# Performance work log

Hardware: AMD Instinct MI355X
Metric: run time of the kernel (lower is better)

Reference implementation:

```python
import jax, jax.numpy as jnp
import numpy as np

B, S, H, DH, D, FD, FU = 4, 256, 12, 64, 768, 2048, 2048


def setup_inputs() -> dict:
    key = jax.random.key(0)
    ks = jax.random.split(key, 12)
    s = 0.02  # typical init scale for weights
    return {
        "resid_pre": jax.random.normal(ks[0], (B, S, D), jnp.float32),
        "ln_scale": jax.random.uniform(ks[1], (B, S, 1), jnp.float32, 0.5, 2.0),
        "probs": jax.nn.softmax(jax.random.normal(ks[2], (B, H, S, S), jnp.float32), axis=-1),
        "W_O": jax.random.normal(ks[3], (H, DH, D), jnp.float32) * s,
        "W_V": jax.random.normal(ks[4], (H, D, DH), jnp.float32) * s,
        "enc_W": jax.random.normal(ks[5], (FD, D), jnp.float32) * s,
        "enc_b": jax.random.normal(ks[6], (FD,), jnp.float32) * s,
        "b_dec": jax.random.normal(ks[7], (D,), jnp.float32) * s,
        "up_dec_W": jax.random.normal(ks[8], (D, FU), jnp.float32) * s,
        "up_b_dec": jax.random.normal(ks[9], (D,), jnp.float32) * s,
        "pruned_features": jax.random.normal(ks[10], (B, S, FU), jnp.float32),
        "connection_mask": jax.random.randint(ks[11], (FD, FU), 0, 2, jnp.int32),
    }


def reference(resid_pre, ln_scale, probs, W_O, W_V, enc_W, enc_b, b_dec,
              up_dec_W, up_b_dec, pruned_features, connection_mask):
    # W_OV: [h, d_model(in), d_model(out)]
    W_OV = jnp.einsum('hko,hmk->hmo', W_O, W_V)
    mask = connection_mask.astype(resid_pre.dtype)

    # --- initial contributions ---
    act_ln = resid_pre / ln_scale                                  # [b,s,d]
    pre_moving = jnp.einsum('bsi,hio,fo->bshf', act_ln, W_OV, enc_W)  # [b,s,h,f_down]
    approx = jnp.einsum('bhqk,bkhf->bqf', probs, pre_moving)       # [b,q,f_down]

    # --- pruned contributions (one upstream AE) ---
    virtual = jnp.einsum('fo,hio,iu->hfu', enc_W, W_OV, up_dec_W) * mask[None]
    up_ln = pruned_features / ln_scale                             # [b,k,f_up]
    post_ov = jnp.einsum('bku,hfu->bhkf', up_ln, virtual)          # [b,h,k,f_down]
    approx = approx + jnp.einsum('bhqk,bhkf->bqf', probs, post_ov)

    # --- bias terms ---
    approx = approx + enc_b[None, None] - (enc_W @ b_dec)[None, None]
    ub_ln = up_b_dec[None, None] / ln_scale                        # [b,s,d]
    ub_post = jnp.einsum('hmd,bsm->bsd', W_OV, ub_ln)              # attn path through OV
    approx = approx + jnp.einsum('fd,bsd->bsf', enc_W, ub_post)
    return approx
```

## Files before the change

kernel.cpp:

```cpp
#include <hip/hip_runtime.h>
#include <hip/hip_bf16.h>
#include <stdint.h>

typedef __bf16 bf16;
typedef __bf16 bf16x8 __attribute__((ext_vector_type(8)));
typedef __bf16 bf16x4 __attribute__((ext_vector_type(4)));
typedef float f32x4 __attribute__((ext_vector_type(4)));

#define AS1 __attribute__((address_space(1)))
#define AS3 __attribute__((address_space(3)))


__device__ __forceinline__ void gld16(const bf16* g, bf16* l) {
  __builtin_amdgcn_global_load_lds((AS1 void*)g, (AS3 void*)l, 16, 0, 0);
}

__global__ void k_sentinel(float* __restrict__ out) {
  int i = blockIdx.x * 256 + threadIdx.x;
  if (i < 2097152) out[i] = 1048576.0f;
}

__global__ void k_prep(const float* __restrict__ lns, float* __restrict__ invln,
                       const float* __restrict__ enc_W, bf16* __restrict__ encWb,
                       const float* __restrict__ probs, bf16* __restrict__ probsT,
                       const int* __restrict__ cmask, bf16* __restrict__ maskb,
                       const float* __restrict__ W_O, bf16* __restrict__ WOb,
                       const float* __restrict__ resid, bf16* __restrict__ Xb,
                       bf16* __restrict__ BgTail, long ldTail) {
  const int bid = blockIdx.x, t = threadIdx.x;
  if (bid < 1) {
    for (int k = 0; k < 4; k++) { int j = t + k * 256; invln[j] = 1.0f / lns[j]; }
  } else if (bid < 1537) {
    long idx = ((long)(bid - 1) * 256 + t) * 4;
    float4 v = *(const float4*)(enc_W + idx);
    bf16x4 o; o[0]=(bf16)v.x; o[1]=(bf16)v.y; o[2]=(bf16)v.z; o[3]=(bf16)v.w;
    *(bf16x4*)(encWb + idx) = o;
  } else if (bid < 4609) {
    long idx = ((long)(bid - 1537) * 256 + t) * 4;
    int s = (int)(idx & 255), q = (int)((idx >> 8) & 255);
    int hb = (int)(idx >> 16), h = hb % 12, b = hb / 12;
    float4 v = *(const float4*)(probs + idx);
    bf16x4 o; o[0]=(bf16)v.x; o[1]=(bf16)v.y; o[2]=(bf16)v.z; o[3]=(bf16)v.w;
    *(bf16x4*)(probsT + (long)b * 786432 + (long)q * 3072 + h * 256 + s) = o;
  } else if (bid < 8705) {
    long idx = ((long)(bid - 4609) * 256 + t) * 4;
    int4 v = *(const int4*)(cmask + idx);
    bf16x4 o; o[0]=(bf16)(float)v.x; o[1]=(bf16)(float)v.y;
    o[2]=(bf16)(float)v.z; o[3]=(bf16)(float)v.w;
    *(bf16x4*)(maskb + idx) = o;
  } else if (bid < 9857) {
    long idx = ((long)(bid - 8705) * 256 + t) * 4;
    int o = (int)(idx % 768), r = (int)((idx / 768) & 127), h = (int)(idx / (768 * 128));
    bf16x4 ov;
    if (r < 64) {
      float4 v = *(const float4*)(W_O + (long)(h * 64 + r) * 768 + o);
      ov[0]=(bf16)v.x; ov[1]=(bf16)v.y; ov[2]=(bf16)v.z; ov[3]=(bf16)v.w;
    } else { ov[0]=ov[1]=ov[2]=ov[3]=(bf16)0.0f; }
    *(bf16x4*)(WOb + idx) = ov;
  } else if (bid < 10625) {
    long idx = ((long)(bid - 9857) * 256 + t) * 4;
    float il = 1.0f / lns[idx / 768];
    float4 v = *(const float4*)(resid + idx);
    bf16x4 o; o[0]=(bf16)(v.x*il); o[1]=(bf16)(v.y*il);
    o[2]=(bf16)(v.z*il); o[3]=(bf16)(v.w*il);
    *(bf16x4*)(Xb + idx) = o;
  } else {
    long idx = ((long)(bid - 10625) * 256 + t) * 4;
    int f = (int)(idx / 768), d = (int)(idx % 768);
    float4 v = *(const float4*)(enc_W + idx);
    bf16x4 o; o[0]=(bf16)v.x; o[1]=(bf16)v.y; o[2]=(bf16)v.z; o[3]=(bf16)v.w;
    *(bf16x4*)(BgTail + (long)f * ldTail + d) = o;
  }
}

__global__ void k_prepT(const float* __restrict__ wv, bf16* __restrict__ WVt,
                        const float* __restrict__ wo, bf16* __restrict__ W_Ot,
                        const float* __restrict__ updW, bf16* __restrict__ updWt,
                        const float* __restrict__ pr, const float* __restrict__ lns,
                        bf16* __restrict__ Ut) {
  __shared__ float tile[32][33];
  const int bid = blockIdx.x;
  int lane = threadIdx.x & 31, rg = threadIdx.x >> 5;
  if (bid < 1152) {
    int r0 = bid;
    int x = r0 % 4, y = (r0 / 4) % 24, h = r0 / 96;
    int k0 = x * 32, i0 = y * 32;
    if (k0 < 64) {
      for (int r = rg; r < 32; r += 8)
        tile[r][lane] = wv[((long)(h * 768 + i0 + r)) * 64 + k0 + lane];
      __syncthreads();
      for (int r = rg; r < 32; r += 8)
        WVt[((long)h * 128 + k0 + r) * 768 + i0 + lane] = (bf16)tile[lane][r];
    } else {
      for (int r = rg; r < 32; r += 8)
        WVt[((long)h * 128 + k0 + r) * 768 + i0 + lane] = (bf16)0.0f;
    }
  } else if (bid < 1728) {
    int r0 = bid - 1152;
    int x = r0 % 2, y = (r0 / 2) % 24, h = r0 / 48;
    int k0 = x * 32, o0 = y * 32;
    for (int r = rg; r < 32; r += 8)
      tile[r][lane] = wo[((long)(h * 64 + k0 + r)) * 768 + o0 + lane];
    __syncthreads();
    for (int r = rg; r < 32; r += 8)
      W_Ot[((long)(h * 768 + o0 + r)) * 64 + k0 + lane] = (bf16)tile[lane][r];
  } else if (bid < 3264) {
    int r0 = bid - 1728;
    int u0 = (r0 % 64) * 32, i0 = (r0 / 64) * 32;
    for (int r = rg; r < 32; r += 8)
      tile[r][lane] = updW[((long)(i0 + r)) * 2048 + u0 + lane];
    __syncthreads();
    for (int r = rg; r < 32; r += 8)
      updWt[((long)(u0 + r)) * 768 + i0 + lane] = (bf16)tile[lane][r];
  } else {
    int r0 = bid - 3264;
    int u0 = (r0 % 64) * 32, s0 = ((r0 / 64) % 8) * 32, b = r0 / 512;
    for (int r = rg; r < 32; r += 8) {
      int s = s0 + r;
      tile[r][lane] = pr[((long)(b * 256 + s)) * 2048 + u0 + lane] *
                      (1.0f / lns[b * 256 + s]);
    }
    __syncthreads();
    for (int r = rg; r < 32; r += 8)
      Ut[((long)b * 2048 + u0 + r) * 256 + s0 + lane] = (bf16)tile[lane][r];
  }
}

__global__ void k_sred(const float* __restrict__ Sp, bf16* __restrict__ dst, long ldd) {
  int i = blockIdx.x * 256 + threadIdx.x;
  if (i < 196608) {
    long idx = (long)i * 4;
    int m = (int)(idx / 768), o = (int)(idx % 768);
    float4 v = *(const float4*)(Sp + idx);
    float4 a = *(const float4*)(Sp + 786432 + idx);
    float4 b = *(const float4*)(Sp + 2 * 786432 + idx);
    float4 c = *(const float4*)(Sp + 3 * 786432 + idx);
    v.x += a.x + b.x + c.x; v.y += a.y + b.y + c.y;
    v.z += a.z + b.z + c.z; v.w += a.w + b.w + c.w;
    bf16x4 ov;
    ov[0] = (bf16)v.x; ov[1] = (bf16)v.y; ov[2] = (bf16)v.z; ov[3] = (bf16)v.w;
    *(bf16x4*)(dst + (long)m * ldd + o) = ov;
  }
}


__device__ __forceinline__ float blk_reduce(float s) {
  __shared__ float red[256];
  red[threadIdx.x] = s; __syncthreads();
  for (int o = 128; o > 0; o >>= 1) {
    if ((int)threadIdx.x < o) red[threadIdx.x] += red[threadIdx.x + o];
    __syncthreads();
  }
  float r = red[0]; __syncthreads();
  return r;
}

__global__ void k_bias_t(const float* __restrict__ W_V, const float* __restrict__ up_b,
                         float* __restrict__ t_hk) {
  int j = blockIdx.x, h = j >> 6, k = j & 63;
  float s = 0.f;
  for (int m = threadIdx.x; m < 768; m += 256)
    s += W_V[((long)(h * 768 + m)) * 64 + k] * up_b[m];
  float r = blk_reduce(s);
  if (threadIdx.x == 0) t_hk[j] = r;
}

__global__ void k_bias_w(const float* __restrict__ W_O, const float* __restrict__ t_hk,
                         float* __restrict__ w) {
  int d = blockIdx.x;
  float s = 0.f;
  for (int j = threadIdx.x; j < 768; j += 256)
    s += W_O[(long)j * 768 + d] * t_hk[j];
  float r = blk_reduce(s);
  if (threadIdx.x == 0) w[d] = r;
}

__global__ void k_bias_c(const float* __restrict__ enc_W, const float* __restrict__ enc_b,
                         const float* __restrict__ b_dec, const float* __restrict__ w,
                         float* __restrict__ c0, float* __restrict__ c1) {
  int f = blockIdx.x;
  float s0 = 0.f, s1 = 0.f;
  for (int d = threadIdx.x; d < 768; d += 256) {
    float e = enc_W[(long)f * 768 + d];
    s0 += e * b_dec[d];
    s1 += e * w[d];
  }
  float r0 = blk_reduce(s0);
  float r1 = blk_reduce(s1);
  if (threadIdx.x == 0) { c0[f] = enc_b[f] - r0; c1[f] = r1; }
}

__global__ __launch_bounds__(256)
void gemm_bt(const bf16* __restrict__ A, const bf16* __restrict__ B, void* __restrict__ Cv,
             int M, int N, int K,
             long lda, long ldb, long ldc,
             int batchH,
             long sa_b, long sa_h, long sb_b, long sb_h, long sc_b, long sc_h,
             int mode, int kChunk,
             const bf16* __restrict__ mask, long mask_ld)
{
  __shared__ __align__(16) bf16 Asm[128 * 64];
  __shared__ __align__(16) bf16 Bsm[128 * 64];

  const int t = threadIdx.x;

  const int nbx = gridDim.x, nby = gridDim.y;
  const int nxy = nbx * nby;
  int orig = blockIdx.x + nbx * blockIdx.y;
  int qq = nxy >> 3, rr = nxy & 7;
  int xcd = orig & 7, lid = orig >> 3;
  int swz = (xcd < rr) ? (xcd * (qq + 1) + lid)
                       : (rr * (qq + 1) + (xcd - rr) * qq + lid);
  const int m0 = (swz % nby) * 128;
  const int n0 = (swz / nby) * 128;

  long aoff, boff, coff;
  int k0, k1;
  if (mode == 4) {
    int z = blockIdx.z;
    int bb = z / batchH, kc = z - bb * batchH;
    aoff = (long)bb * sa_b;
    boff = (long)bb * sb_b;
    coff = (long)bb * sc_b + (long)kc * sc_h;
    k0 = kc * kChunk; k1 = k0 + kChunk; if (k1 > K) k1 = K;
  } else if (mode >= 2) {
    int z = blockIdx.z;
    aoff = 0; boff = 0;
    coff = (long)z * (long)M * ldc;
    k0 = z * kChunk; k1 = k0 + kChunk; if (k1 > K) k1 = K;
  } else {
    int z = blockIdx.z;
    int bb = z / batchH, hh = z - bb * batchH;
    aoff = (long)bb * sa_b + (long)hh * sa_h;
    boff = (long)bb * sb_b + (long)hh * sb_h;
    coff = (long)bb * sc_b + (long)hh * sc_h;
    k0 = 0; k1 = K;
  }

  const bf16* Ab = A + aoff + (long)m0 * lda;
  const bf16* Bb = B + boff + (long)n0 * ldb;

  const int r0 = t >> 3;
  const int g8 = t & 7;

  const int L = t & 63, w = t >> 6;
  const int wm = (w & 1) * 64, wn = (w >> 1) * 64;
  const int r16 = L & 15, q = L >> 4;

  f32x4 acc[4][4];
#pragma unroll
  for (int i = 0; i < 4; i++)
#pragma unroll
    for (int j = 0; j < 4; j++) acc[i][j] = (f32x4){0.f, 0.f, 0.f, 0.f};

  for (int kt = k0; kt < k1; kt += 64) {
#pragma unroll
    for (int j = 0; j < 4; j++) {
      int row = j * 32 + r0;
      int sc = ((g8 ^ (row & 7)) << 3);
      gld16(Ab + (long)row * lda + (kt + sc), &Asm[j * 2048 + t * 8]);
      gld16(Bb + (long)row * ldb + (kt + sc), &Bsm[j * 2048 + t * 8]);
    }
    __syncthreads();

#pragma unroll
    for (int h2 = 0; h2 < 2; h2++) {
      bf16x8 af[4], bfr[4];
#pragma unroll
      for (int i = 0; i < 4; i++) {
        int ra = wm + i * 16 + r16;
        af[i]  = *(const bf16x8*)&Asm[ra * 64 + ((((h2 << 2) + q) ^ (ra & 7)) << 3)];
        int rb = wn + i * 16 + r16;
        bfr[i] = *(const bf16x8*)&Bsm[rb * 64 + ((((h2 << 2) + q) ^ (rb & 7)) << 3)];
      }
#pragma unroll
      for (int mi = 0; mi < 4; mi++)
#pragma unroll
        for (int ni = 0; ni < 4; ni++)
          acc[mi][ni] = __builtin_amdgcn_mfma_f32_16x16x32_bf16(af[mi], bfr[ni], acc[mi][ni], 0, 0, 0);
    }
    __syncthreads();
  }

  if (mode >= 2) {
    float* C = (float*)Cv;
#pragma unroll
    for (int mi = 0; mi < 4; mi++)
#pragma unroll
      for (int ni = 0; ni < 4; ni++)
#pragma unroll
        for (int r = 0; r < 4; r++) {
          int gm = m0 + wm + mi * 16 + q * 4 + r;
          int gn = n0 + wn + ni * 16 + r16;
          long idx = coff + (long)gm * ldc + gn;
          float v = acc[mi][ni][r];
          if (mode == 3) v += C[idx];
          C[idx] = v;
        }
  } else {
    bf16* C = (bf16*)Cv;
#pragma unroll
    for (int mi = 0; mi < 4; mi++)
#pragma unroll
      for (int ni = 0; ni < 4; ni++)
#pragma unroll
        for (int r = 0; r < 4; r++) {
          int gm = m0 + wm + mi * 16 + q * 4 + r;
          int gn = n0 + wn + ni * 16 + r16;
          float v = acc[mi][ni][r];
          if (mode == 1) v *= (float)mask[(long)gm * mask_ld + gn];
          C[coff + (long)gm * ldc + gn] = (bf16)v;
        }
  }
}

__global__ __launch_bounds__(512, 2)
void gemm_fp2(const bf16* __restrict__ A, const bf16* __restrict__ B,
              float* __restrict__ C,
              int M, int N, int K, long lda, long ldb, long ldc,
              int mode, int kChunk)
{
  __shared__ __align__(16) bf16 SM[2][2][16384];

  const int t = threadIdx.x;

  const int nz = gridDim.z;
  int fid = blockIdx.x + gridDim.x * (blockIdx.y + gridDim.y * blockIdx.z);
  const int z  = fid % nz;
  const int t2 = fid / nz;
  const int m0 = (t2 >> 3) * 256;
  const int n0 = (t2 & 7) * 256;

  const long coff = (long)z * (long)M * ldc;
  int k0 = z * kChunk, k1 = k0 + kChunk; if (k1 > K) k1 = K;
  const int NT = (k1 > k0) ? (k1 - k0) >> 6 : 0;

  const bf16* Ab = A + (long)m0 * lda + k0;
  const bf16* Bb = B + (long)n0 * ldb + k0;

  const int sr = t >> 3;
  const int g8 = t & 7;

  const int L = t & 63, w = t >> 6;
  const int wm = (w & 1) * 128;
  const int wn = (w >> 1) * 64;
  const int r16 = L & 15, q = L >> 4;

  f32x4 acc[8][4];
#pragma unroll
  for (int i = 0; i < 8; i++)
#pragma unroll
    for (int j = 0; j < 4; j++) acc[i][j] = (f32x4){0.f, 0.f, 0.f, 0.f};

  auto stage = [&](int tt, int buf) {
    const bf16* Ap = Ab + (long)tt * 64;
    const bf16* Bp = Bb + (long)tt * 64;
#pragma unroll
    for (int j = 0; j < 4; j++) {
      int row = j * 64 + sr;
      int sc = ((g8 ^ (row & 7)) << 3);
      gld16(Ap + (long)row * lda + sc, &SM[buf][0][j * 4096 + t * 8]);
    }
#pragma unroll
    for (int j = 0; j < 4; j++) {
      int row = j * 64 + sr;
      int sc = ((g8 ^ (row & 7)) << 3);
      gld16(Bp + (long)row * ldb + sc, &SM[buf][1][j * 4096 + t * 8]);
    }
  };

  if (NT >= 1) stage(0, 0);

  for (int tt = 0; tt < NT; tt++) {
    if (tt + 1 < NT) {
      stage(tt + 1, (tt + 1) & 1);
      asm volatile("s_waitcnt vmcnt(8)" ::: "memory");
    } else {
      asm volatile("s_waitcnt vmcnt(0)" ::: "memory");
    }
    __builtin_amdgcn_s_barrier();

    const bf16* As = &SM[tt & 1][0][0];
    const bf16* Bs = &SM[tt & 1][1][0];

    bf16x8 a0[4], a1[4], bq0[4], bq1[4];
#pragma unroll
    for (int i = 0; i < 4; i++) {
      int ra = wm + i * 16 + r16;
      a0[i] = *(const bf16x8*)&As[ra * 64 + ((q ^ (ra & 7)) << 3)];
    }
#pragma unroll
    for (int i = 0; i < 4; i++) {
      int rb = wn + i * 16 + r16;
      bq0[i] = *(const bf16x8*)&Bs[rb * 64 + ((q ^ (rb & 7)) << 3)];
    }
#pragma unroll
    for (int i = 0; i < 4; i++) {
      int ra = wm + (4 + i) * 16 + r16;
      a1[i] = *(const bf16x8*)&As[ra * 64 + ((q ^ (ra & 7)) << 3)];
    }
    __builtin_amdgcn_sched_barrier(0);
    __builtin_amdgcn_s_setprio(1);
#pragma unroll
    for (int mi = 0; mi < 4; mi++)
#pragma unroll
      for (int ni = 0; ni < 4; ni++)
        acc[mi][ni] = __builtin_amdgcn_mfma_f32_16x16x32_bf16(a0[mi], bq0[ni], acc[mi][ni], 0, 0, 0);
    __builtin_amdgcn_s_setprio(0);
#pragma unroll
    for (int i = 0; i < 4; i++) {
      int ra = wm + i * 16 + r16;
      a0[i] = *(const bf16x8*)&As[ra * 64 + (((4 + q) ^ (ra & 7)) << 3)];
    }
#pragma unroll
    for (int i = 0; i < 4; i++) {
      int rb = wn + i * 16 + r16;
      bq1[i] = *(const bf16x8*)&Bs[rb * 64 + (((4 + q) ^ (rb & 7)) << 3)];
    }
    __builtin_amdgcn_sched_barrier(0);
    __builtin_amdgcn_s_setprio(1);
#pragma unroll
    for (int mi = 0; mi < 4; mi++)
#pragma unroll
      for (int ni = 0; ni < 4; ni++)
        acc[4 + mi][ni] = __builtin_amdgcn_mfma_f32_16x16x32_bf16(a1[mi], bq0[ni], acc[4 + mi][ni], 0, 0, 0);
    __builtin_amdgcn_s_setprio(0);
#pragma unroll
    for (int i = 0; i < 4; i++) {
      int ra = wm + (4 + i) * 16 + r16;
      a1[i] = *(const bf16x8*)&As[ra * 64 + (((4 + q) ^ (ra & 7)) << 3)];
    }
    __builtin_amdgcn_sched_barrier(0);
    __builtin_amdgcn_s_setprio(1);
#pragma unroll
    for (int mi = 0; mi < 4; mi++)
#pragma unroll
      for (int ni = 0; ni < 4; ni++)
        acc[mi][ni] = __builtin_amdgcn_mfma_f32_16x16x32_bf16(a0[mi], bq1[ni], acc[mi][ni], 0, 0, 0);
    __builtin_amdgcn_s_setprio(0);
    __builtin_amdgcn_sched_barrier(0);
    __builtin_amdgcn_s_setprio(1);
#pragma unroll
    for (int mi = 0; mi < 4; mi++)
#pragma unroll
      for (int ni = 0; ni < 4; ni++)
        acc[4 + mi][ni] = __builtin_amdgcn_mfma_f32_16x16x32_bf16(a1[mi], bq1[ni], acc[4 + mi][ni], 0, 0, 0);
    __builtin_amdgcn_s_setprio(0);

    __builtin_amdgcn_s_barrier();
  }

#pragma unroll
  for (int mi = 0; mi < 8; mi++)
#pragma unroll
    for (int ni = 0; ni < 4; ni++)
#pragma unroll
      for (int r = 0; r < 4; r++) {
        int gm = m0 + wm + mi * 16 + q * 4 + r;
        int gn = n0 + wn + ni * 16 + r16;
        long idx = coff + (long)gm * ldc + gn;
        float v = acc[mi][ni][r];
        if (mode == 3) v += C[idx];
        C[idx] = v;
      }
}

__global__ void k_out(const float* __restrict__ Cp, const float* __restrict__ c0,
                      const float* __restrict__ c1, const float* __restrict__ invln,
                      float* __restrict__ out, int nsplit) {
  int i4 = blockIdx.x * 256 + threadIdx.x;
  long i = (long)i4 * 4;
  int n = (int)(i & 2047), m = (int)(i >> 11);
  float4 v = *(const float4*)(Cp + i);
  for (int z = 1; z < nsplit; z++) {
    float4 u = *(const float4*)(Cp + i + (long)z * 2097152);
    v.x += u.x; v.y += u.y; v.z += u.z; v.w += u.w;
  }
  float il = invln[m];
  float4 a = *(const float4*)(c0 + n);
  float4 b = *(const float4*)(c1 + n);
  v.x += a.x + b.x * il;
  v.y += a.y + b.y * il;
  v.z += a.z + b.z * il;
  v.w += a.w + b.w * il;
  *(float4*)(out + i) = v;
}


extern "C" void kernel_launch(void* const* d_in, const int* in_sizes, int n_in,
                              void* d_out, int out_size, void* d_ws, size_t ws_size,
                              hipStream_t stream) {
  (void)out_size;
  float* out = (float*)d_out;

  int iresid = -1, iln = -1, iprobs = -1, iencb = -1, ipruned = -1, imask = -1;
  int iwo = -1, iwv = -1, iencw = -1, iupdw = -1, ibdec = -1, iupb = -1;
  for (int i = 0; i < n_in; i++) {
    switch (in_sizes[i]) {
      case 786432:  iresid  = i; break;
      case 1024:    iln     = i; break;
      case 3145728: iprobs  = i; break;
      case 2048:    iencb   = i; break;
      case 2097152: ipruned = i; break;
      case 4194304: imask   = i; break;
      case 589824:  if (iwo   < 0) iwo   = i; else iwv   = i; break;
      case 1572864: if (iencw < 0) iencw = i; else iupdw = i; break;
      case 768:     if (ibdec < 0) ibdec = i; else iupb  = i; break;
      default: break;
    }
  }
  bool ok = n_in == 12 && iresid >= 0 && iln >= 0 && iprobs >= 0 && iencb >= 0 &&
            ipruned >= 0 && imask >= 0 && iwo >= 0 && iwv >= 0 && iencw >= 0 &&
            iupdw >= 0 && ibdec >= 0 && iupb >= 0;
  if (!ok) { k_sentinel<<<8192, 256, 0, stream>>>(out); return; }

  const float* resid = (const float*)d_in[iresid];
  const float* lns   = (const float*)d_in[iln];
  const float* probs = (const float*)d_in[iprobs];
  const float* W_O   = (const float*)d_in[iwo];
  const float* W_V   = (const float*)d_in[iwv];
  const float* enc_W = (const float*)d_in[iencw];
  const float* enc_b = (const float*)d_in[iencb];
  const float* b_dec = (const float*)d_in[ibdec];
  const float* updW  = (const float*)d_in[iupdw];
  const float* up_b  = (const float*)d_in[iupb];
  const float* pruned= (const float*)d_in[ipruned];
  const int*   cmask = (const int*)d_in[imask];

  auto pad = [](size_t b) -> size_t { return (b + 255) & ~(size_t)255; };
  const size_t prepB = pad(2359296) + pad(2359296) + pad(3145728) + pad(1572864) +
                       pad(3145728) + pad(1179648) + pad(3145728) + pad(18874368) +
                       pad(12582912);
  const size_t persB = pad(6291456) + pad(4194304) + pad(6291456) + pad(6291456) +
                       pad(8388608) + pad(4096) + pad(3072) + pad(3072) +
                       pad(8192) + pad(8192);
  auto needB = [&](int g, int ns) -> size_t {
    size_t cp = (size_t)ns * 8388608;
    size_t ov = prepB > cp ? prepB : cp;
    long KA = (long)g * 2048 + 768;
    size_t ab = pad((size_t)1024 * KA * 2) + pad((size_t)2048 * KA * 2);
    return ov + persB + ab + (2ull << 20);
  };
  const int cgs[14] = {12, 12, 12, 6, 6, 4, 3, 2, 2, 1, 1, 1, 1, 1};
  const int cns[14] = { 8,  4, 2, 8, 4, 4, 4, 4, 2, 8, 4, 2, 2, 1};
  int gs = 0, nsplit = 0;
  for (int ci = 0; ci < 14; ci++) {
    if (needB(cgs[ci], cns[ci]) <= ws_size) { gs = cgs[ci]; nsplit = cns[ci]; break; }
  }
  if (gs == 0) { gs = 1; nsplit = 1; }

  const long KA = (long)gs * 2048 + 768;

  char* p = (char*)d_ws;
  auto alloc = [&](size_t bytes) -> char* {
    char* r = p; p += (bytes + 255) & ~(size_t)255; return r;
  };
  char* overlayBase = p;
  bf16*  WOb    = (bf16*)alloc(12ull * 128 * 768 * 2);
  bf16*  WVt    = (bf16*)alloc(12ull * 128 * 768 * 2);
  bf16*  updWt  = (bf16*)alloc(2048ull * 768 * 2);
  bf16*  Xb     = (bf16*)alloc(1024ull * 768 * 2);
  bf16*  encWb  = (bf16*)alloc(2048ull * 768 * 2);
  bf16*  W_Ot   = (bf16*)alloc(12ull * 768 * 64 * 2);
  bf16*  T1     = (bf16*)alloc(12ull * 1024 * 128 * 2);
  bf16*  T3     = (bf16*)alloc(4ull * 768 * 3072 * 2);
  float* Sp     = (float*)alloc(4ull * 1024 * 768 * 4);
  {
    size_t used = (size_t)(p - overlayBase);
    size_t cp = (size_t)nsplit * 8388608;
    p = overlayBase + (used > cp ? used : cp);
  }
  float* Cpart  = (float*)overlayBase;
  bf16*  G_t    = (bf16*)alloc(12ull * 2048 * 128 * 2);
  bf16*  Ut     = (bf16*)alloc(4ull * 2048 * 256 * 2);
  bf16*  E1     = (bf16*)alloc(12ull * 2048 * 128 * 2);
  bf16*  probsT = (bf16*)alloc(4ull * 256 * 3072 * 2);
  bf16*  maskb  = (bf16*)alloc(2048ull * 2048 * 2);
  float* invln  = (float*)alloc(1024 * 4);
  float* t_hk   = (float*)alloc(768 * 4);
  float* wv     = (float*)alloc(768 * 4);
  float* c0     = (float*)alloc(2048 * 4);
  float* c1     = (float*)alloc(2048 * 4);
  bf16*  A_g    = (bf16*)alloc((size_t)1024 * KA * 2);
  bf16*  B_g    = (bf16*)alloc((size_t)2048 * KA * 2);

  k_prep<<<12161, 256, 0, stream>>>(lns, invln, enc_W, encWb, probs, probsT,
                                    cmask, maskb, W_O, WOb, resid, Xb,
                                    B_g + (long)gs * 2048, KA);
  k_prepT<<<5312, 256, 0, stream>>>(W_V, WVt, W_O, W_Ot, updW, updWt,
                                    pruned, lns, Ut);
  k_bias_t<<<768, 256, 0, stream>>>(W_V, up_b, t_hk);
  k_bias_w<<<768, 256, 0, stream>>>(W_O, t_hk, wv);
  k_bias_c<<<2048, 256, 0, stream>>>(enc_W, enc_b, b_dec, wv, c0, c1);

  gemm_bt<<<dim3(1, 16, 24), 256, 0, stream>>>(
      encWb, WOb, E1, 2048, 128, 768,
      768, 768, 128, 12,
      (long)(updWt - encWb), 0,
      (long)(WVt - WOb), (long)128 * 768,
      (long)(G_t - E1), (long)2048 * 128,
      0, 0, nullptr, 0);

  gemm_bt<<<dim3(1, 8, 12), 256, 0, stream>>>(
      Xb, WVt, T1, 1024, 128, 768,
      768, 768, 128, 12,
      0, 0, 0, (long)128 * 768, 0, (long)1024 * 128,
      0, 0, nullptr, 0);

  gemm_bt<<<dim3(2, 6, 48), 256, 0, stream>>>(
      W_Ot, T1, T3, 768, 256, 64,
      64, 128, 3072, 12,
      0, (long)768 * 64, (long)256 * 128, (long)1024 * 128, 2359296, 256,
      0, 0, nullptr, 0);

  gemm_bt<<<dim3(6, 2, 16), 256, 0, stream>>>(
      probsT, T3, Sp, 256, 768, 3072,
      3072, 3072, 768, 4,
      786432, 0, 2359296, 0, 196608, 786432,
      4, 768, nullptr, 0);

  k_sred<<<768, 256, 0, stream>>>(Sp, A_g + (long)gs * 2048, KA);

  for (int g = 0; g < 12 / gs; g++) {
    gemm_bt<<<dim3(16, 16, gs), 256, 0, stream>>>(
        E1 + (long)g * gs * 2048 * 128, G_t + (long)g * gs * 2048 * 128, B_g,
        2048, 2048, 64,
        128, 128, KA, gs,
        0, (long)2048 * 128, 0, (long)2048 * 128, 0, 2048,
        1, 0, maskb, 2048);

    gemm_bt<<<dim3(16, 2, 4 * gs), 256, 0, stream>>>(
        probsT + (long)g * gs * 256, Ut, A_g,
        256, 2048, 256,
        3072, 256, KA, gs,
        786432, 256, (long)2048 * 256, 0, 256 * KA, 2048,
        0, 0, nullptr, 0);

    int Kthis = (g == 0) ? (int)KA : gs * 2048;
    int kc = ((Kthis / nsplit + 63) / 64) * 64;
    gemm_fp2<<<dim3(8, 4, nsplit), 512, 0, stream>>>(
        A_g, B_g, Cpart,
        1024, 2048, Kthis,
        KA, KA, 2048,
        (g == 0) ? 2 : 3, kc);
  }

  k_out<<<2048, 256, 0, stream>>>(Cpart, c0, c1, invln, out, nsplit);
}
```

Baseline: 436.5 us.

## Stage bf16 GEMM epilogue through LDS for vectorized stores; simplify fp2 inner loop

```diff
diff --git a/kernel.cpp b/kernel.cpp
--- a/kernel.cpp
+++ b/kernel.cpp
@@ -199,8 +199,9 @@
              int mode, int kChunk,
              const bf16* __restrict__ mask, long mask_ld)
 {
-  __shared__ __align__(16) bf16 Asm[128 * 64];
-  __shared__ __align__(16) bf16 Bsm[128 * 64];
+  __shared__ __align__(16) bf16 SMEM[16384];
+  bf16* Asm = SMEM;
+  bf16* Bsm = SMEM + 8192;
 
   const int t = threadIdx.x;
 
@@ -299,18 +300,38 @@
         }
   } else {
     bf16* C = (bf16*)Cv;
-#pragma unroll
-    for (int mi = 0; mi < 4; mi++)
-#pragma unroll
-      for (int ni = 0; ni < 4; ni++)
-#pragma unroll
-        for (int r = 0; r < 4; r++) {
-          int gm = m0 + wm + mi * 16 + q * 4 + r;
-          int gn = n0 + wn + ni * 16 + r16;
-          float v = acc[mi][ni][r];
-          if (mode == 1) v *= (float)mask[(long)gm * mask_ld + gn];
-          C[coff + (long)gm * ldc + gn] = (bf16)v;
+    bf16* lbuf = SMEM;
+    const int lrbase = (wm >> 6) * 32 + q * 4;
+    const int lr_r = t >> 2;
+    const int colg = (t & 3) * 32;
+#pragma unroll
+    for (int hh = 0; hh < 2; hh++) {
+#pragma unroll
+      for (int m2 = 0; m2 < 2; m2++) {
+        int mi = hh * 2 + m2;
+#pragma unroll
+        for (int ni = 0; ni < 4; ni++) {
+          int col = wn + ni * 16 + r16;
+#pragma unroll
+          for (int r = 0; r < 4; r++)
+            lbuf[(lrbase + m2 * 16 + r) * 136 + col] = (bf16)acc[mi][ni][r];
         }
+      }
+      __syncthreads();
+      int gm = m0 + (lr_r >> 5) * 64 + hh * 32 + (lr_r & 31);
+#pragma unroll
+      for (int s = 0; s < 4; s++) {
+        bf16x8 v = *(const bf16x8*)&lbuf[lr_r * 136 + colg + 8 * s];
+        int gn = n0 + colg + 8 * s;
+        if (mode == 1) {
+          bf16x8 mv = *(const bf16x8*)&mask[(long)gm * mask_ld + gn];
+#pragma unroll
+          for (int j = 0; j < 8; j++) v[j] = (bf16)((float)v[j] * (float)mv[j]);
+        }
+        *(bf16x8*)&C[coff + (long)gm * ldc + gn] = v;
+      }
+      __syncthreads();
+    }
   }
 }
 
@@ -382,71 +403,25 @@
 
     const bf16* As = &SM[tt & 1][0][0];
     const bf16* Bs = &SM[tt & 1][1][0];
-
-    bf16x8 a0[4], a1[4], bq0[4], bq1[4];
-#pragma unroll
-    for (int i = 0; i < 4; i++) {
-      int ra = wm + i * 16 + r16;
-      a0[i] = *(const bf16x8*)&As[ra * 64 + ((q ^ (ra & 7)) << 3)];
-    }
-#pragma unroll
-    for (int i = 0; i < 4; i++) {
-      int rb = wn + i * 16 + r16;
-      bq0[i] = *(const bf16x8*)&Bs[rb * 64 + ((q ^ (rb & 7)) << 3)];
-    }
-#pragma unroll
-    for (int i = 0; i < 4; i++) {
-      int ra = wm + (4 + i) * 16 + r16;
-      a1[i] = *(const bf16x8*)&As[ra * 64 + ((q ^ (ra & 7)) << 3)];
-    }
-    __builtin_amdgcn_sched_barrier(0);
-    __builtin_amdgcn_s_setprio(1);
-#pragma unroll
-    for (int mi = 0; mi < 4; mi++)
-#pragma unroll
-      for (int ni = 0; ni < 4; ni++)
-        acc[mi][ni] = __builtin_amdgcn_mfma_f32_16x16x32_bf16(a0[mi], bq0[ni], acc[mi][ni], 0, 0, 0);
-    __builtin_amdgcn_s_setprio(0);
-#pragma unroll
-    for (int i = 0; i < 4; i++) {
-      int ra = wm + i * 16 + r16;
-      a0[i] = *(const bf16x8*)&As[ra * 64 + (((4 + q) ^ (ra & 7)) << 3)];
-    }
-#pragma unroll
-    for (int i = 0; i < 4; i++) {
-      int rb = wn + i * 16 + r16;
-      bq1[i] = *(const bf16x8*)&Bs[rb * 64 + (((4 + q) ^ (rb & 7)) << 3)];
-    }
-    __builtin_amdgcn_sched_barrier(0);
-    __builtin_amdgcn_s_setprio(1);
-#pragma unroll
-    for (int mi = 0; mi < 4; mi++)
-#pragma unroll
-      for (int ni = 0; ni < 4; ni++)
-        acc[4 + mi][ni] = __builtin_amdgcn_mfma_f32_16x16x32_bf16(a1[mi], bq0[ni], acc[4 + mi][ni], 0, 0, 0);
-    __builtin_amdgcn_s_setprio(0);
-#pragma unroll
-    for (int i = 0; i < 4; i++) {
-      int ra = wm + (4 + i) * 16 + r16;
-      a1[i] = *(const bf16x8*)&As[ra * 64 + (((4 + q) ^ (ra & 7)) << 3)];
-    }
-    __builtin_amdgcn_sched_barrier(0);
-    __builtin_amdgcn_s_setprio(1);
-#pragma unroll
-    for (int mi = 0; mi < 4; mi++)
-#pragma unroll
-      for (int ni = 0; ni < 4; ni++)
-        acc[mi][ni] = __builtin_amdgcn_mfma_f32_16x16x32_bf16(a0[mi], bq1[ni], acc[mi][ni], 0, 0, 0);
-    __builtin_amdgcn_s_setprio(0);
-    __builtin_amdgcn_sched_barrier(0);
-    __builtin_amdgcn_s_setprio(1);
-#pragma unroll
-    for (int mi = 0; mi < 4; mi++)
-#pragma unroll
-      for (int ni = 0; ni < 4; ni++)
-        acc[4 + mi][ni] = __builtin_amdgcn_mfma_f32_16x16x32_bf16(a1[mi], bq1[ni], acc[4 + mi][ni], 0, 0, 0);
-    __builtin_amdgcn_s_setprio(0);
-
+#pragma unroll
+    for (int h2 = 0; h2 < 2; h2++) {
+      bf16x8 af[8], bfr[4];
+#pragma unroll
+      for (int i = 0; i < 8; i++) {
+        int ra = wm + i * 16 + r16;
+        af[i]  = *(const bf16x8*)&As[ra * 64 + ((((h2 << 2) + q) ^ (ra & 7)) << 3)];
+      }
+#pragma unroll
+      for (int i = 0; i < 4; i++) {
+        int rb = wn + i * 16 + r16;
+        bfr[i] = *(const bf16x8*)&Bs[rb * 64 + ((((h2 << 2) + q) ^ (rb & 7)) << 3)];
+      }
+#pragma unroll
+      for (int mi = 0; mi < 8; mi++)
+#pragma unroll
+        for (int ni = 0; ni < 4; ni++)
+          acc[mi][ni] = __builtin_amdgcn_mfma_f32_16x16x32_bf16(af[mi], bfr[ni], acc[mi][ni], 0, 0, 0);
+    }
     __builtin_amdgcn_s_barrier();
   }
 
```

After: 406.7 us. -6.8%, faster.
